# Kernel optimization log

Hardware: AMD Instinct MI355X
Metric: run time of the kernel (lower is better)

## Reference

```python
import jax, jax.numpy as jnp
import numpy as np

NUM_EXPERTS = 8
CAPACITY_FACTOR = 1.0
MIN_CAPACITY = 4


def setup_inputs() -> dict:
    key = jax.random.key(0)
    k0, k1, k2, k3 = jax.random.split(key, 4)
    B, S, M, F, E = 4, 2048, 2048, 8192, NUM_EXPERTS
    return {
        "hidden_states": jax.random.normal(k0, (B, S, M), jnp.float32),
        "wg": jax.random.normal(k1, (M, E), jnp.float32) * 0.02,
        "w1": jax.random.normal(k2, (E, M, F), jnp.float32) * 0.02,
        "b1": jnp.zeros((E, F), jnp.float32),
        "w2": jax.random.normal(k3, (E, F, M), jnp.float32) * 0.02,
        "b2": jnp.zeros((E, M), jnp.float32),
    }


def reference(hidden_states, wg, w1, b1, w2, b2):
    B, S, M = hidden_states.shape
    E = NUM_EXPERTS
    T = B * S  # total tokens
    x = hidden_states.reshape(T, M)

    # ---- top-1 gating (DeepSpeed top1gating, no noise / no RTS) ----
    logits = x @ wg                                  # [T, E]
    gates = jax.nn.softmax(logits, axis=-1)          # [T, E]
    capacity = max(int(np.ceil(T / E * CAPACITY_FACTOR)), MIN_CAPACITY)

    idx1 = jnp.argmax(gates, axis=1)                 # [T]
    mask1 = jax.nn.one_hot(idx1, E, dtype=gates.dtype)  # [T, E]

    # position of each token within its expert's queue
    locations1 = jnp.cumsum(mask1, axis=0) - 1.0     # [T, E]

    # load-balancing aux loss (computed before capacity drop)
    me = jnp.mean(gates, axis=0)
    ce = jnp.mean(mask1, axis=0)
    l_aux = jnp.sum(me * ce) * E

    # drop tokens beyond capacity
    mask1 = mask1 * (locations1 < capacity).astype(mask1.dtype)
    locations1_s = jnp.sum(locations1 * mask1, axis=1).astype(jnp.int32)  # [T]

    gates1 = gates * mask1                           # [T, E], zero for dropped tokens
    loc_sc = jax.nn.one_hot(locations1_s, capacity, dtype=gates.dtype)    # [T, C]

    combine_weights = jnp.einsum("se,sc->sec", gates1, loc_sc)            # [T, E, C]
    dispatch_mask = (combine_weights > 0).astype(x.dtype)                  # [T, E, C]

    # ---- dispatch -> grouped-GEMM experts -> combine ----
    dispatched = jnp.einsum("sec,sm->ecm", dispatch_mask, x)              # [E, C, M]
    h = jax.nn.gelu(jnp.einsum("ecm,emf->ecf", dispatched, w1) + b1[:, None, :])
    expert_out = jnp.einsum("ecf,efm->ecm", h, w2) + b2[:, None, :]       # [E, C, M]

    out = jnp.einsum("sec,ecm->sm", combine_weights, expert_out)          # [T, M]
    return out.reshape(B, S, M), l_aux
```

## Files before the change

### kernel.cpp

```cpp
#include <hip/hip_runtime.h>
#include <hip/hip_bf16.h>
#include <math.h>

#define T_TOK 8192
#define M_DIM 2048
#define F_DIM 8192
#define E_NUM 8
#define CAP   1024

typedef unsigned short u16;
typedef __attribute__((ext_vector_type(8))) short short8;
typedef __attribute__((ext_vector_type(4))) float f32x4;

__device__ __forceinline__ u16 f2bf(float f){
  unsigned int x = __builtin_bit_cast(unsigned int, f);
  unsigned int lsb = (x >> 16) & 1u;
  x += 0x7fffu + lsb;
  return (u16)(x >> 16);
}
__device__ __forceinline__ unsigned int pack2(float a, float b){
  return (unsigned int)f2bf(a) | ((unsigned int)f2bf(b) << 16);
}

typedef __attribute__((address_space(3))) unsigned int lds_uint;
typedef __attribute__((address_space(1))) const unsigned int g_uint;
__device__ __forceinline__ void gl_lds16(const u16* g, u16* l){
  __builtin_amdgcn_global_load_lds((g_uint*)g, (lds_uint*)l, 16, 0, 0);
}

__device__ __forceinline__ float gelu_tanh(float v){
  float u = 0.7978845608028654f * (v + 0.044715f * v * v * v);
  return 0.5f * v * (1.0f + tanhf(u));
}

__global__ __launch_bounds__(256) void gating_kernel(
    const float* __restrict__ x, const float* __restrict__ wg,
    int* __restrict__ expert_id, float* __restrict__ gate_val,
    float* __restrict__ mepart)
{
  int wave = threadIdx.x >> 6, lane = threadIdx.x & 63;
  int t = blockIdx.x * 4 + wave;
  float acc[8];
  #pragma unroll
  for (int e = 0; e < 8; ++e) acc[e] = 0.f;
  const float* xr = x + (size_t)t * M_DIM;
  for (int i = lane; i < M_DIM; i += 64) {
    float xv = xr[i];
    const float4* wr = (const float4*)(wg + (size_t)i * 8);
    float4 w0 = wr[0], w1v = wr[1];
    acc[0] += xv * w0.x;  acc[1] += xv * w0.y;  acc[2] += xv * w0.z;  acc[3] += xv * w0.w;
    acc[4] += xv * w1v.x; acc[5] += xv * w1v.y; acc[6] += xv * w1v.z; acc[7] += xv * w1v.w;
  }
  #pragma unroll
  for (int off = 32; off; off >>= 1)
    #pragma unroll
    for (int e = 0; e < 8; ++e) acc[e] += __shfl_xor(acc[e], off);

  float mx = acc[0]; int bi = 0;
  #pragma unroll
  for (int e = 1; e < 8; ++e) if (acc[e] > mx) { mx = acc[e]; bi = e; }
  float p[8]; float s = 0.f;
  #pragma unroll
  for (int e = 0; e < 8; ++e) { p[e] = expf(acc[e] - mx); s += p[e]; }
  float inv = 1.f / s;

  __shared__ float pl[4][8];
  if (lane == 0) {
    expert_id[t] = bi;
    gate_val[t] = p[bi] * inv;
    #pragma unroll
    for (int e = 0; e < 8; ++e) pl[wave][e] = p[e] * inv;
  }
  __syncthreads();
  if (threadIdx.x < 8) {
    float m = pl[0][threadIdx.x] + pl[1][threadIdx.x] + pl[2][threadIdx.x] + pl[3][threadIdx.x];
    mepart[blockIdx.x * 8 + threadIdx.x] = m;
  }
}

__global__ __launch_bounds__(1024) void scan_kernel(
    const int* __restrict__ expert_id, const float* __restrict__ gate_val,
    const float* __restrict__ mepart, int nmep,
    int* __restrict__ slot_token, float* __restrict__ slot_gate,
    float* __restrict__ laux_out)
{
  __shared__ int wcnt[16][8];
  __shared__ int base[8];
  __shared__ float red[128][8];
  int tid = threadIdx.x, wave = tid >> 6, lane = tid & 63;
  if (tid < 8) base[tid] = 0;

  int e0 = tid & 7, g = tid >> 3;
  float mesum = 0.f;
  for (int r = g; r < nmep; r += 128) mesum += mepart[r * 8 + e0];
  red[g][e0] = mesum;
  __syncthreads();

  for (int tile = 0; tile < T_TOK / 1024; ++tile) {
    int t = tile * 1024 + tid;
    int e = expert_id[t];
    int lp = 0;
    #pragma unroll
    for (int ee = 0; ee < 8; ++ee) {
      unsigned long long m = __ballot(e == ee);
      if (lane == 0) wcnt[wave][ee] = __popcll(m);
      if (ee == e)   lp = __popcll(m & ((1ull << lane) - 1ull));
    }
    __syncthreads();
    int wp = 0;
    for (int w2 = 0; w2 < wave; ++w2) wp += wcnt[w2][e];
    int pos = base[e] + wp + lp;
    if (pos < CAP) {
      slot_token[e * CAP + pos] = t;
      slot_gate[e * CAP + pos] = gate_val[t];
    }
    __syncthreads();
    if (tid < 8) {
      int s = 0;
      for (int w2 = 0; w2 < 16; ++w2) s += wcnt[w2][tid];
      base[tid] += s;
    }
    __syncthreads();
  }

  if (tid < 8) {
    float me = 0.f;
    for (int r = 0; r < 128; ++r) me += red[r][tid];
    me /= (float)T_TOK;
    float ce = (float)base[tid] / (float)T_TOK;
    red[0][tid] = me * ce;
  }
  __syncthreads();
  if (tid == 0) {
    float s = 0.f;
    for (int e = 0; e < 8; ++e) s += red[0][e];
    *laux_out = s * (float)E_NUM;
  }
}

__global__ __launch_bounds__(256) void transpose_cvt_kernel(
    const float* __restrict__ in, u16* __restrict__ out, int R, int Cc)
{
  __shared__ float tile[64][65];
  size_t off = (size_t)blockIdx.z * R * Cc;
  const float* ine = in + off;
  u16* oute = out + off;
  int r0 = blockIdx.y * 64, c0 = blockIdx.x * 64;
  int tr = threadIdx.x >> 4, tc = threadIdx.x & 15;
  #pragma unroll
  for (int it = 0; it < 4; ++it) {
    float4 v = *(const float4*)&ine[(size_t)(r0 + it * 16 + tr) * Cc + c0 + tc * 4];
    tile[it * 16 + tr][tc * 4 + 0] = v.x;
    tile[it * 16 + tr][tc * 4 + 1] = v.y;
    tile[it * 16 + tr][tc * 4 + 2] = v.z;
    tile[it * 16 + tr][tc * 4 + 3] = v.w;
  }
  __syncthreads();
  int oc = threadIdx.x >> 2, q = threadIdx.x & 3;
  u16 vals[16];
  #pragma unroll
  for (int i = 0; i < 16; ++i) vals[i] = f2bf(tile[q * 16 + i][oc]);
  unsigned int w[8];
  #pragma unroll
  for (int i = 0; i < 8; ++i) w[i] = (unsigned int)vals[2 * i] | ((unsigned int)vals[2 * i + 1] << 16);
  u16* orow = oute + (size_t)(c0 + oc) * R + r0 + q * 16;
  uint4 p0; p0.x = w[0]; p0.y = w[1]; p0.z = w[2]; p0.w = w[3];
  uint4 p1; p1.x = w[4]; p1.y = w[5]; p1.z = w[6]; p1.w = w[7];
  *(uint4*)orow = p0;
  *(uint4*)(orow + 8) = p1;
}

__global__ __launch_bounds__(256) void dispatch_kernel(
    const float* __restrict__ x, const int* __restrict__ slot_token,
    u16* __restrict__ Xe)
{
  int slot = blockIdx.x;
  int t = slot_token[slot];
  int c0 = threadIdx.x * 8;
  uint4 pk;
  if (t < 0) {
    pk.x = pk.y = pk.z = pk.w = 0u;
  } else {
    const float* xr = x + (size_t)t * M_DIM + c0;
    float4 a = *(const float4*)xr;
    float4 b = *(const float4*)(xr + 4);
    pk.x = pack2(a.x, a.y); pk.y = pack2(a.z, a.w);
    pk.z = pack2(b.x, b.y); pk.w = pack2(b.z, b.w);
  }
  *(uint4*)(Xe + (size_t)slot * M_DIM + c0) = pk;
}

template<int MH, int GATE>
__device__ __forceinline__ void do_phase(
    const u16* __restrict__ ab, const u16* __restrict__ bb,
    int arow_base, int brow_base,
    short8 (&bfr)[4], f32x4 (&acc)[8][4],
    const u16* __restrict__ smat, u16* sreg, int skt, int skh, int K,
    int sg, int srow, int wave)
{
  short8 af[4];
  #pragma unroll
  for (int m2 = 0; m2 < 4; ++m2)
    af[m2] = *(const short8*)&ab[arow_base + (MH * 4 + m2) * 512];
  if (MH == 0) {
    #pragma unroll
    for (int n2 = 0; n2 < 4; ++n2)
      bfr[n2] = *(const short8*)&bb[brow_base + n2 * 512];
  }
  const u16* src = smat + (size_t)skt * 64 + skh * 32 + sg * 8;
  #pragma unroll
  for (int j = 0; j < 2; ++j)
    gl_lds16(src + (size_t)(srow + j * 128) * K, sreg + (j * 512 + (wave << 6)) * 8);
  __builtin_amdgcn_s_barrier();
  asm volatile("s_waitcnt lgkmcnt(0)" ::: "memory");
  __builtin_amdgcn_sched_barrier(0);
  __builtin_amdgcn_s_setprio(1);
  #pragma unroll
  for (int m2 = 0; m2 < 4; ++m2)
    #pragma unroll
    for (int n2 = 0; n2 < 4; ++n2)
      acc[MH * 4 + m2][n2] = __builtin_amdgcn_mfma_f32_16x16x32_bf16(
          af[m2], bfr[n2], acc[MH * 4 + m2][n2], 0, 0, 0);
  __builtin_amdgcn_s_setprio(0);
  __builtin_amdgcn_sched_barrier(0);
  if (GATE) {
    asm volatile("s_waitcnt vmcnt(8)" ::: "memory");
    __builtin_amdgcn_sched_barrier(0);
  }
  __builtin_amdgcn_s_barrier();
}

template<int EPI>
__global__ __launch_bounds__(512, 2) void gemm8_kernel(
    const u16* __restrict__ A,
    const u16* __restrict__ B,
    const float* __restrict__ bias,
    u16* __restrict__ Hout,
    float* __restrict__ Out,
    const int* __restrict__ slot_token, const float* __restrict__ slot_gate,
    int K, int NR)
{
  __shared__ u16 SA[2][2][8192];
  __shared__ u16 SB[2][2][8192];

  int e = blockIdx.z;
  int n0 = blockIdx.x * 256, m0 = blockIdx.y * 256;
  const u16* Ae = A + (size_t)e * CAP * K + (size_t)m0 * K;
  const u16* Be = B + (size_t)e * NR * K + (size_t)n0 * K;

  int tid = threadIdx.x, wave = tid >> 6, lane = tid & 63;
  int wr = wave >> 2, wc = wave & 3;
  int l15 = lane & 15, g2 = lane >> 4;

  int sg   = (tid & 3) ^ ((tid >> 3) & 3);
  int srow = tid >> 2;
  int rs = (l15 >> 1) & 3;
  int cg = (g2 ^ rs) * 8;
  int arow_base = (wr * 128 + l15) * 32 + cg;
  int brow_base = (wc * 64 + l15) * 32 + cg;

  f32x4 acc[8][4];
  #pragma unroll
  for (int m = 0; m < 8; ++m)
    #pragma unroll
    for (int n = 0; n < 4; ++n)
      acc[m][n] = (f32x4){0.f, 0.f, 0.f, 0.f};
  short8 bfr[4];

  auto stage0 = [&](const u16* mat, u16* region, int kt, int kh) {
    const u16* src = mat + (size_t)kt * 64 + kh * 32 + sg * 8;
    #pragma unroll
    for (int j = 0; j < 2; ++j)
      gl_lds16(src + (size_t)(srow + j * 128) * K, region + (j * 512 + (wave << 6)) * 8);
  };

  int nk = K >> 6, ni = nk >> 1;
  stage0(Ae, &SA[0][0][0], 0, 0); stage0(Be, &SB[0][0][0], 0, 0);
  stage0(Ae, &SA[0][1][0], 0, 1); stage0(Be, &SB[0][1][0], 0, 1);
  stage0(Ae, &SA[1][0][0], 1, 0); stage0(Be, &SB[1][0][0], 1, 0);
  asm volatile("s_waitcnt vmcnt(8)" ::: "memory");
  __builtin_amdgcn_sched_barrier(0);
  __builtin_amdgcn_s_barrier();

  #pragma unroll 1
  for (int i = 0; i < ni; ++i) {
    int s1 = 2 * i + 1;
    int s2 = 2 * i + 2 < nk ? 2 * i + 2 : nk - 1;
    int s3 = 2 * i + 3 < nk ? 2 * i + 3 : nk - 1;
    do_phase<0,0>(&SA[0][0][0], &SB[0][0][0], arow_base, brow_base, bfr, acc,
                  Ae, &SA[1][1][0], s1, 1, K, sg, srow, wave);
    do_phase<1,1>(&SA[0][0][0], &SB[0][0][0], arow_base, brow_base, bfr, acc,
                  Be, &SB[1][1][0], s1, 1, K, sg, srow, wave);
    do_phase<0,0>(&SA[0][1][0], &SB[0][1][0], arow_base, brow_base, bfr, acc,
                  Ae, &SA[0][0][0], s2, 0, K, sg, srow, wave);
    do_phase<1,1>(&SA[0][1][0], &SB[0][1][0], arow_base, brow_base, bfr, acc,
                  Be, &SB[0][0][0], s2, 0, K, sg, srow, wave);
    do_phase<0,0>(&SA[1][0][0], &SB[1][0][0], arow_base, brow_base, bfr, acc,
                  Ae, &SA[0][1][0], s2, 1, K, sg, srow, wave);
    do_phase<1,1>(&SA[1][0][0], &SB[1][0][0], arow_base, brow_base, bfr, acc,
                  Be, &SB[0][1][0], s2, 1, K, sg, srow, wave);
    do_phase<0,0>(&SA[1][1][0], &SB[1][1][0], arow_base, brow_base, bfr, acc,
                  Ae, &SA[1][0][0], s3, 0, K, sg, srow, wave);
    do_phase<1,1>(&SA[1][1][0], &SB[1][1][0], arow_base, brow_base, bfr, acc,
                  Be, &SB[1][0][0], s3, 0, K, sg, srow, wave);
  }

  int wrb = wr * 128, wcb = wc * 64;
  const float* be = bias + (size_t)e * NR + n0;
  if (EPI == 0) {
    #pragma unroll
    for (int wm = 0; wm < 8; ++wm) {
      #pragma unroll
      for (int j = 0; j < 4; ++j) {
        int r = wrb + wm * 16 + g2 * 4 + j;
        size_t rowoff = (size_t)e * CAP * F_DIM + (size_t)(m0 + r) * F_DIM + n0;
        #pragma unroll
        for (int n = 0; n < 4; ++n) {
          int c = wcb + n * 16 + l15;
          float v = acc[wm][n][j] + be[c];
          Hout[rowoff + c] = f2bf(gelu_tanh(v));
        }
      }
    }
  } else {
    #pragma unroll
    for (int wm = 0; wm < 8; ++wm) {
      #pragma unroll
      for (int j = 0; j < 4; ++j) {
        int r = wrb + wm * 16 + g2 * 4 + j;
        int slot = e * CAP + m0 + r;
        int tk = slot_token[slot];
        if (tk >= 0) {
          float gv = slot_gate[slot];
          size_t rowoff = (size_t)tk * M_DIM + n0;
          #pragma unroll
          for (int n = 0; n < 4; ++n) {
            int c = wcb + n * 16 + l15;
            Out[rowoff + c] = gv * (acc[wm][n][j] + be[c]);
          }
        }
      }
    }
  }
}

extern "C" void kernel_launch(void* const* d_in, const int* in_sizes, int n_in,
                              void* d_out, int out_size, void* d_ws, size_t ws_size,
                              hipStream_t stream) {
  const float* x  = (const float*)d_in[0];
  const float* wg = (const float*)d_in[1];
  const float* w1 = (const float*)d_in[2];
  const float* b1 = (const float*)d_in[3];
  const float* w2 = (const float*)d_in[4];
  const float* b2 = (const float*)d_in[5];
  float* out = (float*)d_out;

  char* ws = (char*)d_ws;
  size_t o = 0;
  auto alloc = [&](size_t bytes) -> void* {
    void* p = ws + o;
    o += (bytes + 255) & ~(size_t)255;
    return p;
  };
  u16*   w1T        = (u16*)  alloc((size_t)E_NUM * F_DIM * M_DIM * 2);
  u16*   w2T        = (u16*)  alloc((size_t)E_NUM * M_DIM * F_DIM * 2);
  u16*   h          = (u16*)  alloc((size_t)E_NUM * CAP * F_DIM * 2);
  u16*   Xe         = (u16*)  alloc((size_t)E_NUM * CAP * M_DIM * 2);
  int*   expert_id  = (int*)  alloc(T_TOK * 4);
  float* gate_val   = (float*)alloc(T_TOK * 4);
  int*   slot_token = (int*)  alloc(E_NUM * CAP * 4);
  float* slot_gate  = (float*)alloc(E_NUM * CAP * 4);
  float* mepart     = (float*)alloc(2048 * 8 * 4);

  hipMemsetAsync(d_out, 0, (size_t)out_size * 4, stream);
  hipMemsetAsync(slot_token, 0xFF, E_NUM * CAP * 4, stream);

  gating_kernel<<<T_TOK / 4, 256, 0, stream>>>(x, wg, expert_id, gate_val, mepart);
  scan_kernel<<<1, 1024, 0, stream>>>(expert_id, gate_val, mepart, 2048,
                                      slot_token, slot_gate, out + (out_size - 1));
  transpose_cvt_kernel<<<dim3(128, 32, 8), 256, 0, stream>>>(w1, w1T, 2048, 8192);
  transpose_cvt_kernel<<<dim3(32, 128, 8), 256, 0, stream>>>(w2, w2T, 8192, 2048);
  dispatch_kernel<<<E_NUM * CAP, 256, 0, stream>>>(x, slot_token, Xe);
  gemm8_kernel<0><<<dim3(F_DIM / 256, CAP / 256, E_NUM), 512, 0, stream>>>(
      Xe, w1T, b1, h, nullptr, nullptr, nullptr, M_DIM, F_DIM);
  gemm8_kernel<1><<<dim3(M_DIM / 256, CAP / 256, E_NUM), 512, 0, stream>>>(
      h, w2T, b2, nullptr, out, slot_token, slot_gate, F_DIM, M_DIM);
}
```

Measured before the change: 1.082 ms.

## Prefetch next A fragments from LDS during MFMA and drop a barrier per phase

Software-pipelines the LDS-to-register reads for the A operand: each phase now loads the next phase's A fragments (ping-ponging between two register sets) while the current fragments feed the MFMAs. It waits only on the older LDS reads (lgkmcnt(4)) instead of draining all of them, and removes the barrier that sat before the MFMA block. The vmcnt wait is now done in every phase instead of every other one. The aim is to hide LDS read latency behind matrix math, at the cost of more VGPRs and tighter reasoning about whether buffers are overwritten before they are read across waves.

```diff
diff --git a/kernel.cpp b/kernel.cpp
--- a/kernel.cpp
+++ b/kernel.cpp
@@ -190,29 +190,31 @@
   *(uint4*)(Xe + (size_t)slot * M_DIM + c0) = pk;
 }
 
-template<int MH, int GATE>
+template<int MH>
 __device__ __forceinline__ void do_phase(
-    const u16* __restrict__ ab, const u16* __restrict__ bb,
+    short8 (&afC)[4], short8 (&afN)[4], short8 (&bfr)[4],
+    const u16* __restrict__ bb,
+    const u16* __restrict__ abN,
     int arow_base, int brow_base,
-    short8 (&bfr)[4], f32x4 (&acc)[8][4],
+    f32x4 (&acc)[8][4],
     const u16* __restrict__ smat, u16* sreg, int skt, int skh, int K,
     int sg, int srow, int wave)
 {
-  short8 af[4];
-  #pragma unroll
-  for (int m2 = 0; m2 < 4; ++m2)
-    af[m2] = *(const short8*)&ab[arow_base + (MH * 4 + m2) * 512];
+  constexpr int MHN = 1 - MH;
   if (MH == 0) {
     #pragma unroll
     for (int n2 = 0; n2 < 4; ++n2)
       bfr[n2] = *(const short8*)&bb[brow_base + n2 * 512];
-  }
+    __builtin_amdgcn_sched_barrier(0);
+  }
+  #pragma unroll
+  for (int m2 = 0; m2 < 4; ++m2)
+    afN[m2] = *(const short8*)&abN[arow_base + (MHN * 4 + m2) * 512];
   const u16* src = smat + (size_t)skt * 64 + skh * 32 + sg * 8;
   #pragma unroll
   for (int j = 0; j < 2; ++j)
     gl_lds16(src + (size_t)(srow + j * 128) * K, sreg + (j * 512 + (wave << 6)) * 8);
-  __builtin_amdgcn_s_barrier();
-  asm volatile("s_waitcnt lgkmcnt(0)" ::: "memory");
+  asm volatile("s_waitcnt lgkmcnt(4)" ::: "memory");
   __builtin_amdgcn_sched_barrier(0);
   __builtin_amdgcn_s_setprio(1);
   #pragma unroll
@@ -220,13 +222,10 @@
     #pragma unroll
     for (int n2 = 0; n2 < 4; ++n2)
       acc[MH * 4 + m2][n2] = __builtin_amdgcn_mfma_f32_16x16x32_bf16(
-          af[m2], bfr[n2], acc[MH * 4 + m2][n2], 0, 0, 0);
+          afC[m2], bfr[n2], acc[MH * 4 + m2][n2], 0, 0, 0);
   __builtin_amdgcn_s_setprio(0);
   __builtin_amdgcn_sched_barrier(0);
-  if (GATE) {
-    asm volatile("s_waitcnt vmcnt(8)" ::: "memory");
-    __builtin_amdgcn_sched_barrier(0);
-  }
+  asm volatile("s_waitcnt vmcnt(8)" ::: "memory");
   __builtin_amdgcn_s_barrier();
 }
 
@@ -265,7 +264,7 @@
     #pragma unroll
     for (int n = 0; n < 4; ++n)
       acc[m][n] = (f32x4){0.f, 0.f, 0.f, 0.f};
-  short8 bfr[4];
+  short8 afX[4], afY[4], bfr[4];
 
   auto stage0 = [&](const u16* mat, u16* region, int kt, int kh) {
     const u16* src = mat + (size_t)kt * 64 + kh * 32 + sg * 8;
@@ -281,28 +280,31 @@
   asm volatile("s_waitcnt vmcnt(8)" ::: "memory");
   __builtin_amdgcn_sched_barrier(0);
   __builtin_amdgcn_s_barrier();
+  #pragma unroll
+  for (int m2 = 0; m2 < 4; ++m2)
+    afX[m2] = *(const short8*)&SA[0][0][arow_base + m2 * 512];
 
   #pragma unroll 1
   for (int i = 0; i < ni; ++i) {
     int s1 = 2 * i + 1;
     int s2 = 2 * i + 2 < nk ? 2 * i + 2 : nk - 1;
     int s3 = 2 * i + 3 < nk ? 2 * i + 3 : nk - 1;
-    do_phase<0,0>(&SA[0][0][0], &SB[0][0][0], arow_base, brow_base, bfr, acc,
-                  Ae, &SA[1][1][0], s1, 1, K, sg, srow, wave);
-    do_phase<1,1>(&SA[0][0][0], &SB[0][0][0], arow_base, brow_base, bfr, acc,
-                  Be, &SB[1][1][0], s1, 1, K, sg, srow, wave);
-    do_phase<0,0>(&SA[0][1][0], &SB[0][1][0], arow_base, brow_base, bfr, acc,
-                  Ae, &SA[0][0][0], s2, 0, K, sg, srow, wave);
-    do_phase<1,1>(&SA[0][1][0], &SB[0][1][0], arow_base, brow_base, bfr, acc,
-                  Be, &SB[0][0][0], s2, 0, K, sg, srow, wave);
-    do_phase<0,0>(&SA[1][0][0], &SB[1][0][0], arow_base, brow_base, bfr, acc,
-                  Ae, &SA[0][1][0], s2, 1, K, sg, srow, wave);
-    do_phase<1,1>(&SA[1][0][0], &SB[1][0][0], arow_base, brow_base, bfr, acc,
-                  Be, &SB[0][1][0], s2, 1, K, sg, srow, wave);
-    do_phase<0,0>(&SA[1][1][0], &SB[1][1][0], arow_base, brow_base, bfr, acc,
-                  Ae, &SA[1][0][0], s3, 0, K, sg, srow, wave);
-    do_phase<1,1>(&SA[1][1][0], &SB[1][1][0], arow_base, brow_base, bfr, acc,
-                  Be, &SB[1][0][0], s3, 0, K, sg, srow, wave);
+    do_phase<0>(afX, afY, bfr, &SB[0][0][0], &SA[0][0][0], arow_base, brow_base, acc,
+                Ae, &SA[1][1][0], s1, 1, K, sg, srow, wave);
+    do_phase<1>(afY, afX, bfr, &SB[0][0][0], &SA[0][1][0], arow_base, brow_base, acc,
+                Be, &SB[1][1][0], s1, 1, K, sg, srow, wave);
+    do_phase<0>(afX, afY, bfr, &SB[0][1][0], &SA[0][1][0], arow_base, brow_base, acc,
+                Ae, &SA[0][0][0], s2, 0, K, sg, srow, wave);
+    do_phase<1>(afY, afX, bfr, &SB[0][1][0], &SA[1][0][0], arow_base, brow_base, acc,
+                Be, &SB[0][0][0], s2, 0, K, sg, srow, wave);
+    do_phase<0>(afX, afY, bfr, &SB[1][0][0], &SA[1][0][0], arow_base, brow_base, acc,
+                Ae, &SA[0][1][0], s2, 1, K, sg, srow, wave);
+    do_phase<1>(afY, afX, bfr, &SB[1][0][0], &SA[1][1][0], arow_base, brow_base, acc,
+                Be, &SB[0][1][0], s2, 1, K, sg, srow, wave);
+    do_phase<0>(afX, afY, bfr, &SB[1][1][0], &SA[1][1][0], arow_base, brow_base, acc,
+                Ae, &SA[1][0][0], s3, 0, K, sg, srow, wave);
+    do_phase<1>(afY, afX, bfr, &SB[1][1][0], &SA[0][0][0], arow_base, brow_base, acc,
+                Be, &SB[1][0][0], s3, 0, K, sg, srow, wave);
   }
 
   int wrb = wr * 128, wcb = wc * 64;
```

New measurement: 1.094 ms. Within noise of the previous version (+1.0%).

## Prefetch B tiles earlier in GEMM pipeline and swizzle workgroup order

Applied to the files above, without the earlier changes.

Restructures the LDS ring schedule so B-matrix tiles are loaded one half-phase earlier than A tiles (B is read once per phase pair, before its MH==1 slot is overwritten). The prologue now also stages SB[1][1], and the wait counts drop to vmcnt(6). Adds a workgroup-ID swizzle that interleaves blocks in groups of 8, spreading neighbouring tiles across XCDs for cache locality. Removing the sched_barriers lets the compiler move instructions more freely, but the schedule must stay race-free.

```diff
diff --git a/kernel.cpp b/kernel.cpp
--- a/kernel.cpp
+++ b/kernel.cpp
@@ -192,21 +192,21 @@
 
 template<int MH, int GATE>
 __device__ __forceinline__ void do_phase(
-    const u16* __restrict__ ab, const u16* __restrict__ bb,
+    const u16* __restrict__ aReg, const u16* __restrict__ bReg,
     int arow_base, int brow_base,
     short8 (&bfr)[4], f32x4 (&acc)[8][4],
     const u16* __restrict__ smat, u16* sreg, int skt, int skh, int K,
     int sg, int srow, int wave)
 {
   short8 af[4];
+  if (MH == 0) {
+    #pragma unroll
+    for (int n2 = 0; n2 < 4; ++n2)
+      bfr[n2] = *(const short8*)&bReg[brow_base + n2 * 512];
+  }
   #pragma unroll
   for (int m2 = 0; m2 < 4; ++m2)
-    af[m2] = *(const short8*)&ab[arow_base + (MH * 4 + m2) * 512];
-  if (MH == 0) {
-    #pragma unroll
-    for (int n2 = 0; n2 < 4; ++n2)
-      bfr[n2] = *(const short8*)&bb[brow_base + n2 * 512];
-  }
+    af[m2] = *(const short8*)&aReg[arow_base + (MH * 4 + m2) * 512];
   const u16* src = smat + (size_t)skt * 64 + skh * 32 + sg * 8;
   #pragma unroll
   for (int j = 0; j < 2; ++j)
@@ -222,11 +222,8 @@
       acc[MH * 4 + m2][n2] = __builtin_amdgcn_mfma_f32_16x16x32_bf16(
           af[m2], bfr[n2], acc[MH * 4 + m2][n2], 0, 0, 0);
   __builtin_amdgcn_s_setprio(0);
-  __builtin_amdgcn_sched_barrier(0);
-  if (GATE) {
-    asm volatile("s_waitcnt vmcnt(8)" ::: "memory");
-    __builtin_amdgcn_sched_barrier(0);
-  }
+  if (GATE)
+    asm volatile("s_waitcnt vmcnt(6)" ::: "memory");
   __builtin_amdgcn_s_barrier();
 }
 
@@ -243,8 +240,16 @@
   __shared__ u16 SA[2][2][8192];
   __shared__ u16 SB[2][2][8192];
 
-  int e = blockIdx.z;
-  int n0 = blockIdx.x * 256, m0 = blockIdx.y * 256;
+  int orig = blockIdx.x + gridDim.x * (blockIdx.y + gridDim.y * blockIdx.z);
+  int nwg  = gridDim.x * gridDim.y * gridDim.z;
+  int swz  = (orig & 7) * (nwg >> 3) + (orig >> 3);
+  int gxy  = gridDim.x * gridDim.y;
+  int e    = swz / gxy;
+  int rem  = swz - e * gxy;
+  int by   = rem / gridDim.x;
+  int bx   = rem - by * gridDim.x;
+  int n0 = bx * 256, m0 = by * 256;
+
   const u16* Ae = A + (size_t)e * CAP * K + (size_t)m0 * K;
   const u16* Be = B + (size_t)e * NR * K + (size_t)n0 * K;
 
@@ -275,34 +280,37 @@
   };
 
   int nk = K >> 6, ni = nk >> 1;
-  stage0(Ae, &SA[0][0][0], 0, 0); stage0(Be, &SB[0][0][0], 0, 0);
-  stage0(Ae, &SA[0][1][0], 0, 1); stage0(Be, &SB[0][1][0], 0, 1);
-  stage0(Ae, &SA[1][0][0], 1, 0); stage0(Be, &SB[1][0][0], 1, 0);
-  asm volatile("s_waitcnt vmcnt(8)" ::: "memory");
-  __builtin_amdgcn_sched_barrier(0);
+  stage0(Be, &SB[0][0][0], 0, 0);
+  stage0(Ae, &SA[0][0][0], 0, 0);
+  stage0(Be, &SB[0][1][0], 0, 1);
+  stage0(Ae, &SA[0][1][0], 0, 1);
+  stage0(Be, &SB[1][0][0], 1, 0);
+  stage0(Ae, &SA[1][0][0], 1, 0);
+  stage0(Be, &SB[1][1][0], 1, 1);
+  asm volatile("s_waitcnt vmcnt(6)" ::: "memory");
   __builtin_amdgcn_s_barrier();
 
   #pragma unroll 1
   for (int i = 0; i < ni; ++i) {
-    int s1 = 2 * i + 1;
-    int s2 = 2 * i + 2 < nk ? 2 * i + 2 : nk - 1;
-    int s3 = 2 * i + 3 < nk ? 2 * i + 3 : nk - 1;
+    int t1 = 2 * i + 1;
+    int t2 = 2 * i + 2 < nk ? 2 * i + 2 : nk - 1;
+    int t3 = 2 * i + 3 < nk ? 2 * i + 3 : nk - 1;
     do_phase<0,0>(&SA[0][0][0], &SB[0][0][0], arow_base, brow_base, bfr, acc,
-                  Ae, &SA[1][1][0], s1, 1, K, sg, srow, wave);
-    do_phase<1,1>(&SA[0][0][0], &SB[0][0][0], arow_base, brow_base, bfr, acc,
-                  Be, &SB[1][1][0], s1, 1, K, sg, srow, wave);
+                  Ae, &SA[1][1][0], t1, 1, K, sg, srow, wave);
+    do_phase<1,0>(&SA[0][0][0], &SB[0][0][0], arow_base, brow_base, bfr, acc,
+                  Be, &SB[0][0][0], t2, 0, K, sg, srow, wave);
     do_phase<0,0>(&SA[0][1][0], &SB[0][1][0], arow_base, brow_base, bfr, acc,
-                  Ae, &SA[0][0][0], s2, 0, K, sg, srow, wave);
+                  Ae, &SA[0][0][0], t2, 0, K, sg, srow, wave);
     do_phase<1,1>(&SA[0][1][0], &SB[0][1][0], arow_base, brow_base, bfr, acc,
-                  Be, &SB[0][0][0], s2, 0, K, sg, srow, wave);
+                  Be, &SB[0][1][0], t2, 1, K, sg, srow, wave);
     do_phase<0,0>(&SA[1][0][0], &SB[1][0][0], arow_base, brow_base, bfr, acc,
-                  Ae, &SA[0][1][0], s2, 1, K, sg, srow, wave);
-    do_phase<1,1>(&SA[1][0][0], &SB[1][0][0], arow_base, brow_base, bfr, acc,
-                  Be, &SB[0][1][0], s2, 1, K, sg, srow, wave);
+                  Ae, &SA[0][1][0], t2, 1, K, sg, srow, wave);
+    do_phase<1,0>(&SA[1][0][0], &SB[1][0][0], arow_base, brow_base, bfr, acc,
+                  Be, &SB[1][0][0], t3, 0, K, sg, srow, wave);
     do_phase<0,0>(&SA[1][1][0], &SB[1][1][0], arow_base, brow_base, bfr, acc,
-                  Ae, &SA[1][0][0], s3, 0, K, sg, srow, wave);
+                  Ae, &SA[1][0][0], t3, 0, K, sg, srow, wave);
     do_phase<1,1>(&SA[1][1][0], &SB[1][1][0], arow_base, brow_base, bfr, acc,
-                  Be, &SB[1][0][0], s3, 0, K, sg, srow, wave);
+                  Be, &SB[1][1][0], t3, 1, K, sg, srow, wave);
   }
 
   int wrb = wr * 128, wcb = wc * 64;
```

Result: faster. 1.045 ms (-3.4%).
